# Performance work log

Hardware: AMD Instinct MI355X
Metric: run time of the kernel (lower is better)

## Reference

```python
import jax, jax.numpy as jnp
import numpy as np

B, L, D, H = 8, 1500, 1024, 8
HD = D // H
N_BOUNDARIES = 300  # exactly 300 boundaries per sequence -> max_segments = 300
EPS = 1e-5


def setup_inputs() -> dict:
    key = jax.random.key(0)
    ks = jax.random.split(key, 6)
    rng = np.random.default_rng(0)
    boundaries = np.zeros((B, L), dtype=np.float32)
    for b in range(B):
        boundaries[b, rng.permutation(L)[:N_BOUNDARIES]] = 1.0
    lengths = rng.uniform(0.5, 1.0, size=(B,)).astype(np.float32)
    hidden = jax.random.normal(ks[0], (B, L, D), jnp.float32)
    learned_query = jax.random.normal(ks[1], (D,), jnp.float32) * 0.02
    eye = jnp.eye(D, dtype=jnp.float32)
    # identity-initialized projections, perturbed so the test is non-trivial
    Wk = eye + 0.02 * jax.random.normal(ks[2], (D, D), jnp.float32)
    Wv = eye + 0.02 * jax.random.normal(ks[3], (D, D), jnp.float32)
    Wo = eye + 0.02 * jax.random.normal(ks[4], (D, D), jnp.float32)
    return {
        'hidden': hidden,
        'boundaries': jnp.asarray(boundaries),
        'lengths': jnp.asarray(lengths),
        'learned_query': learned_query,
        'Wk': Wk, 'Wv': Wv, 'Wo': Wo,
        'ln_gamma': jnp.ones((D,), jnp.float32),
        'ln_beta': jnp.zeros((D,), jnp.float32),
        'max_segments': N_BOUNDARIES,
    }


def _attention_pooling(hidden, boundaries, lengths, learned_query, Wk, Wv, Wo,
                       ln_gamma, ln_beta, max_segments):
    # segment id per token: cumsum(b) - b (token before first boundary -> seg 0)
    seg_id = jnp.cumsum(boundaries, axis=1) - boundaries            # (B, L)
    # foo[b,t,s] = s - seg_id[b,t]; foo == 0 -> token t belongs to segment s
    seg_mask = (jnp.arange(max_segments)[None, None, :] == seg_id[:, :, None])
    actual_lens = (lengths * L).astype(jnp.int32)                   # (B,)
    len_mask = jnp.arange(L)[None, :] < actual_lens[:, None]        # (B, L)
    seg_mask = seg_mask & len_mask[:, :, None]                      # (B, L, S) bool

    # LayerNorm (biased variance, as torch.nn.LayerNorm)
    mu = jnp.mean(hidden, axis=-1, keepdims=True)
    var = jnp.var(hidden, axis=-1, keepdims=True)
    hn = (hidden - mu) * jax.lax.rsqrt(var + EPS) * ln_gamma + ln_beta

    k = (hn @ Wk.T).reshape(B, L, H, HD)
    v = (hn @ Wv.T).reshape(B, L, H, HD)
    q = learned_query.reshape(H, HD)
    # queries are the same learned vector for every segment -> compute (B,H,L)
    # once and broadcast across S (same math as the original dense matmul)
    scores = jnp.einsum('hd,blhd->bhl', q, k) * (HD ** -0.5)        # (B, H, L)

    mask = seg_mask.transpose(0, 2, 1)[:, None, :, :]               # (B, 1, S, L)
    scores4 = jnp.where(mask, scores[:, :, None, :], -1e30)         # (B, H, S, L)
    w = jax.nn.softmax(scores4, axis=-1)
    w = jnp.where(mask, w, 0.0)
    # rows with no valid token: softmax of all -inf -> nan_to_num(0) in torch
    row_valid = jnp.any(mask, axis=-1, keepdims=True)
    w = jnp.where(row_valid, w, 0.0)

    pooled = jnp.einsum('bhsl,blhd->bshd', w, v).reshape(B, max_segments, D)
    return pooled @ Wo.T                                            # (B, S, D)


def reference(hidden, boundaries, lengths, learned_query, Wk, Wv, Wo,
              ln_gamma, ln_beta, max_segments):
    return _attention_pooling(hidden, boundaries, lengths, learned_query,
                              Wk, Wv, Wo, ln_gamma, ln_beta, max_segments)
```

## Files before the change

### kernel.cpp

```cpp
#include <hip/hip_runtime.h>
#include <hip/hip_bf16.h>

#define BPK_B 8
#define BPK_L 1500
#define BPK_D 1024
#define BPK_H 8
#define BPK_S 300
#define BPK_EPS 1e-5f
#define BPK_M (BPK_B * BPK_L)
#define BPK_MS (BPK_B * BPK_S)
#define BPK_MS_TILES 19
#define BPK_HP_ROWS 2432
#define BPK_PO_PAD 3072

typedef __hip_bfloat16 bf16;
typedef __bf16 bf16x8 __attribute__((ext_vector_type(8)));
typedef float v4f __attribute__((ext_vector_type(4)));

static __device__ __forceinline__ float bf_lo(unsigned u) {
    return __uint_as_float((u & 0xffffu) << 16);
}
static __device__ __forceinline__ float bf_hi(unsigned u) {
    return __uint_as_float((u >> 16) << 16);
}
static __device__ __forceinline__ void bpk_store(float v, float* p) { *p = v; }
static __device__ __forceinline__ void bpk_store(float v, bf16* p) { *p = __float2bfloat16(v); }
static __device__ __forceinline__ uint2 pack4bf(float a, float b, float c, float d) {
    union { bf16 h[4]; uint2 u; } pk;
    pk.h[0] = __float2bfloat16(a); pk.h[1] = __float2bfloat16(b);
    pk.h[2] = __float2bfloat16(c); pk.h[3] = __float2bfloat16(d);
    return pk.u;
}

#define BPK_GL2LDS(gsrc, ldst)                                                 \
    __builtin_amdgcn_global_load_lds(                                          \
        (const __attribute__((address_space(1))) void*)(gsrc),                 \
        (__attribute__((address_space(3))) void*)(ldst), 16, 0, 0)

__global__ __launch_bounds__(256) void bpk_prep_kernel(
    const float* __restrict__ Wv, const float* __restrict__ Wo,
    const float* __restrict__ lq, const float* __restrict__ Wk,
    const float* __restrict__ boundaries, const float* __restrict__ lengths,
    bf16* __restrict__ wvb, bf16* __restrict__ wob, bf16* __restrict__ qkb,
    int* __restrict__ seg_start, int* __restrict__ seg_cnt) {
    __shared__ unsigned char flags[1536];
    __shared__ int st_sh[BPK_S + 2];
    __shared__ int wsumi[4];
    int blk = blockIdx.x;
    int tid = threadIdx.x;
    if (blk < 2048) {
        const float* s = blk < 1024 ? Wv : Wo;
        bf16* d = blk < 1024 ? wvb : wob;
        int i = ((blk & 1023) * 256 + tid) * 4;
        float4 v = *(const float4*)(s + i);
        *(uint2*)(d + i) = pack4bf(v.x, v.y, v.z, v.w);
        return;
    }
    if (blk < 2080) {
        int o = (blk - 2048) * 256 + tid;
        int h = o >> 10, k = o & 1023;
        const float* wr = Wk + (size_t)(h * 128) * BPK_D + k;
        const float* qr = lq + h * 128;
        float s = 0.f;
        #pragma unroll 8
        for (int d = 0; d < 128; d++)
            s += qr[d] * wr[(size_t)d * BPK_D];
        qkb[o] = __float2bfloat16(s);
        return;
    }
    int b = blk - 2080;
    int alen = (int)(lengths[b] * (float)BPK_L);
    const float* bd = boundaries + (size_t)b * BPK_L;
    for (int t = tid; t < 1536; t += 256)
        flags[t] = (t < BPK_L && bd[t] >= 0.5f) ? 1 : 0;
    for (int s = tid; s < BPK_S + 2; s += 256) st_sh[s] = BPK_L;
    __syncthreads();
    int base = tid * 6;
    int lsum = 0;
    #pragma unroll
    for (int j = 0; j < 6; j++) lsum += flags[base + j];
    int lane = tid & 63, wid = tid >> 6;
    int scan = lsum;
    #pragma unroll
    for (int off = 1; off < 64; off <<= 1) {
        int u = __shfl_up(scan, off);
        if (lane >= off) scan += u;
    }
    if (lane == 63) wsumi[wid] = scan;
    __syncthreads();
    int wbase = 0;
    for (int w = 0; w < wid; w++) wbase += wsumi[w];
    int run = wbase + scan - lsum;
    #pragma unroll
    for (int j = 0; j < 6; j++) {
        int t = base + j;
        if (t < BPK_L) {
            int sid = run;
            if ((t == 0 || flags[t - 1]) && sid <= BPK_S) st_sh[sid] = t;
            if (flags[t]) run++;
        }
    }
    __syncthreads();
    for (int s = tid; s < BPK_S; s += 256) {
        int st = st_sh[s];
        int e = min(st_sh[s + 1], alen);
        int s0 = min(st, alen);
        seg_start[b * BPK_S + s] = st;
        seg_cnt[b * BPK_S + s] = max(0, e - s0);
    }
}

__global__ __launch_bounds__(256) void bpk_ln_score_kernel(
    const float* __restrict__ x, const float* __restrict__ gamma,
    const float* __restrict__ beta, const bf16* __restrict__ qkb,
    float2* __restrict__ murs, float* __restrict__ scores) {
    __shared__ bf16 qks[BPK_H * BPK_D];
    int tid = threadIdx.x;
    int lane = tid & 63, wid = tid >> 6;
    for (int i = tid; i < (BPK_H * BPK_D) / 8; i += 256)
        ((uint4*)qks)[i] = ((const uint4*)qkb)[i];
    float4 g[4], bb[4];
    #pragma unroll
    for (int j = 0; j < 4; j++) {
        g[j]  = *(const float4*)(gamma + j * 256 + lane * 4);
        bb[j] = *(const float4*)(beta + j * 256 + lane * 4);
    }
    __syncthreads();
    const int nwaves = gridDim.x * 4;
    for (int row = blockIdx.x * 4 + wid; row < BPK_M; row += nwaves) {
        const float* xr = x + (size_t)row * BPK_D;
        float4 f[4];
        float s = 0.f, sq = 0.f;
        #pragma unroll
        for (int j = 0; j < 4; j++) {
            f[j] = *(const float4*)(xr + j * 256 + lane * 4);
            s  += f[j].x + f[j].y + f[j].z + f[j].w;
            sq += f[j].x * f[j].x + f[j].y * f[j].y
                + f[j].z * f[j].z + f[j].w * f[j].w;
        }
        #pragma unroll
        for (int off = 1; off < 64; off <<= 1) {
            s  += __shfl_xor(s, off);
            sq += __shfl_xor(sq, off);
        }
        float mu = s * (1.0f / BPK_D);
        float var = sq * (1.0f / BPK_D) - mu * mu;
        float rs = rsqrtf(var + BPK_EPS);
        float hv[16];
        #pragma unroll
        for (int j = 0; j < 4; j++) {
            hv[j * 4 + 0] = (f[j].x - mu) * rs * g[j].x + bb[j].x;
            hv[j * 4 + 1] = (f[j].y - mu) * rs * g[j].y + bb[j].y;
            hv[j * 4 + 2] = (f[j].z - mu) * rs * g[j].z + bb[j].z;
            hv[j * 4 + 3] = (f[j].w - mu) * rs * g[j].w + bb[j].w;
        }
        float p[8];
        #pragma unroll
        for (int h = 0; h < 8; h++) {
            p[h] = 0.f;
            #pragma unroll
            for (int j = 0; j < 4; j++) {
                uint2 qv = *(const uint2*)(qks + h * BPK_D + j * 256 + lane * 4);
                p[h] += hv[j * 4 + 0] * bf_lo(qv.x) + hv[j * 4 + 1] * bf_hi(qv.x)
                      + hv[j * 4 + 2] * bf_lo(qv.y) + hv[j * 4 + 3] * bf_hi(qv.y);
            }
        }
        #pragma unroll
        for (int h = 0; h < 8; h++)
            #pragma unroll
            for (int off = 1; off < 64; off <<= 1)
                p[h] += __shfl_xor(p[h], off);
        if (lane < 8) {
            int b = row / BPK_L, t = row - b * BPK_L;
            scores[((size_t)b * BPK_H + lane) * BPK_L + t] =
                p[lane] * 0.088388347648318447f;
        } else if (lane == 8) {
            murs[row] = make_float2(mu, rs);
        }
    }
}

__global__ __launch_bounds__(256) void bpk_pool_kernel(
    const float* __restrict__ scores, const float* __restrict__ x,
    const float* __restrict__ gamma, const float* __restrict__ beta,
    const float2* __restrict__ murs,
    const int* __restrict__ seg_start, const int* __restrict__ seg_cnt,
    bf16* __restrict__ hpool) {
    int bs = blockIdx.x;
    int b = bs / BPK_S;
    int tid = threadIdx.x;
    int lane = tid & 63, wid = tid >> 6;
    __shared__ float minv[8][2];
    __shared__ float wls[8][128];
    int cnt = seg_cnt[bs], st = seg_start[bs];
    float4 g4 = *(const float4*)(gamma + tid * 4);
    float4 b4 = *(const float4*)(beta + tid * 4);
    float acc[8][4];
    #pragma unroll
    for (int h = 0; h < 8; h++)
        #pragma unroll
        for (int j = 0; j < 4; j++) acc[h][j] = 0.f;
    if (cnt > 0) {
        if (wid == 0) {
            int h = lane & 7, i0 = lane >> 3;
            const float* sc = scores + ((size_t)(b * 8 + h)) * BPK_L + st;
            float m = -1e30f;
            for (int i = i0; i < cnt; i += 8) m = fmaxf(m, sc[i]);
            #pragma unroll
            for (int off = 8; off < 64; off <<= 1) m = fmaxf(m, __shfl_xor(m, off));
            float l = 0.f;
            for (int i = i0; i < cnt; i += 8) l += __expf(sc[i] - m);
            #pragma unroll
            for (int off = 8; off < 64; off <<= 1) l += __shfl_xor(l, off);
            if (i0 == 0) { minv[h][0] = m; minv[h][1] = 1.0f / l; }
        }
        __syncthreads();
        for (int cb = 0; cb < cnt; cb += 128) {
            int cc = min(128, cnt - cb);
            int hh = tid >> 5, i0 = (tid & 31) * 4;
            #pragma unroll
            for (int j = 0; j < 4; j++) {
                int i = i0 + j;
                if (i < cc)
                    wls[hh][i] = __expf(scores[((size_t)(b * 8 + hh)) * BPK_L + st + cb + i]
                                        - minv[hh][0]) * minv[hh][1];
            }
            __syncthreads();
            const float* xp = x + (size_t)(b * BPK_L + st + cb) * BPK_D + tid * 4;
            const float2* mp = murs + (size_t)(b * BPK_L + st + cb);
            for (int i = 0; i < cc; i++) {
                float4 f = *(const float4*)(xp + (size_t)i * BPK_D);
                float2 mr = mp[i];
                float x0 = (f.x - mr.x) * mr.y * g4.x + b4.x;
                float x1 = (f.y - mr.x) * mr.y * g4.y + b4.y;
                float x2 = (f.z - mr.x) * mr.y * g4.z + b4.z;
                float x3 = (f.w - mr.x) * mr.y * g4.w + b4.w;
                #pragma unroll
                for (int h = 0; h < 8; h++) {
                    float w = wls[h][i];
                    acc[h][0] += w * x0; acc[h][1] += w * x1;
                    acc[h][2] += w * x2; acc[h][3] += w * x3;
                }
            }
            __syncthreads();
        }
    }
    #pragma unroll
    for (int h = 0; h < 8; h++)
        *(uint2*)(hpool + ((size_t)h * BPK_HP_ROWS + bs) * BPK_D + tid * 4) =
            pack4bf(acc[h][0], acc[h][1], acc[h][2], acc[h][3]);
}

__global__ __launch_bounds__(256) void bpk_headgemm_kernel(
    const bf16* __restrict__ hpool, const bf16* __restrict__ wvb,
    bf16* __restrict__ pooled) {
    const int mt = blockIdx.x, h = blockIdx.y;
    const int m0 = mt * 128;
    const bf16* A = hpool + (size_t)h * BPK_HP_ROWS * BPK_D;
    const bf16* W = wvb + (size_t)(h * 128) * BPK_D;
    __shared__ bf16 As[128][32];
    __shared__ bf16 Bs[128][32];
    const int tid = threadIdx.x;
    const int lane = tid & 63, wid = tid >> 6;
    const int wm = (wid & 1) * 64, wn = (wid >> 1) * 64;
    const int lm = lane & 15, quad = lane >> 4;
    const int c0 = wid * 2;
    const int rA = c0 * 16 + (lane >> 2);
    const int colc = (lane & 3) * 8;

    v4f acc[4][4];
    #pragma unroll
    for (int i = 0; i < 4; i++)
        #pragma unroll
        for (int j = 0; j < 4; j++) acc[i][j] = (v4f){0.f, 0.f, 0.f, 0.f};

    for (int k0 = 0; k0 < BPK_D; k0 += 32) {
        const bf16* pa = &A[(size_t)(m0 + rA) * BPK_D + k0 + colc];
        const bf16* pw = &W[(size_t)rA * BPK_D + k0 + colc];
        BPK_GL2LDS(pa, &As[c0 * 16][0]);
        BPK_GL2LDS(pa + (size_t)16 * BPK_D, &As[(c0 + 1) * 16][0]);
        BPK_GL2LDS(pw, &Bs[c0 * 16][0]);
        BPK_GL2LDS(pw + (size_t)16 * BPK_D, &Bs[(c0 + 1) * 16][0]);
        __syncthreads();
        bf16x8 af[4], bfr[4];
        #pragma unroll
        for (int i = 0; i < 4; i++)
            af[i] = *(const bf16x8*)&As[wm + i * 16 + lm][quad * 8];
        #pragma unroll
        for (int j = 0; j < 4; j++)
            bfr[j] = *(const bf16x8*)&Bs[wn + j * 16 + lm][quad * 8];
        #pragma unroll
        for (int i = 0; i < 4; i++)
            #pragma unroll
            for (int j = 0; j < 4; j++)
                acc[i][j] = __builtin_amdgcn_mfma_f32_16x16x32_bf16(af[i], bfr[j], acc[i][j], 0, 0, 0);
        __syncthreads();
    }
    #pragma unroll
    for (int i = 0; i < 4; i++) {
        int mbase = m0 + wm + i * 16 + quad * 4;
        #pragma unroll
        for (int j = 0; j < 4; j++) {
            int col = h * 128 + wn + j * 16 + lm;
            #pragma unroll
            for (int r = 0; r < 4; r++) {
                int m = mbase + r;
                if (m < BPK_MS)
                    pooled[(size_t)m * BPK_D + col] = __float2bfloat16(acc[i][j][r]);
            }
        }
    }
}

template <typename OT>
__global__ __launch_bounds__(256) void bpk_gemm_bt_kernel(
    const bf16* __restrict__ A, const bf16* __restrict__ W,
    OT* __restrict__ O, int M, int NT) {
    const int flat = blockIdx.x;
    const int xcd = flat & 7, slot = flat >> 3;
    const int mt = xcd + 8 * (slot / NT);
    const int nt = slot % NT;
    const int n0 = nt * 128;
    const int m0 = mt * 128;
    __shared__ bf16 As[128][32];
    __shared__ bf16 Bs[128][32];
    const int tid = threadIdx.x;
    const int lane = tid & 63, wid = tid >> 6;
    const int wm = (wid & 1) * 64, wn = (wid >> 1) * 64;
    const int lm = lane & 15, quad = lane >> 4;
    const int c0 = wid * 2;
    const int rA = c0 * 16 + (lane >> 2);
    const int colc = (lane & 3) * 8;

    v4f acc[4][4];
    #pragma unroll
    for (int i = 0; i < 4; i++)
        #pragma unroll
        for (int j = 0; j < 4; j++) acc[i][j] = (v4f){0.f, 0.f, 0.f, 0.f};

    for (int k0 = 0; k0 < BPK_D; k0 += 32) {
        const bf16* pa = &A[(size_t)(m0 + rA) * BPK_D + k0 + colc];
        const bf16* pw = &W[(size_t)(n0 + rA) * BPK_D + k0 + colc];
        BPK_GL2LDS(pa, &As[c0 * 16][0]);
        BPK_GL2LDS(pa + (size_t)16 * BPK_D, &As[(c0 + 1) * 16][0]);
        BPK_GL2LDS(pw, &Bs[c0 * 16][0]);
        BPK_GL2LDS(pw + (size_t)16 * BPK_D, &Bs[(c0 + 1) * 16][0]);
        __syncthreads();
        bf16x8 af[4], bfr[4];
        #pragma unroll
        for (int i = 0; i < 4; i++)
            af[i] = *(const bf16x8*)&As[wm + i * 16 + lm][quad * 8];
        #pragma unroll
        for (int j = 0; j < 4; j++)
            bfr[j] = *(const bf16x8*)&Bs[wn + j * 16 + lm][quad * 8];
        #pragma unroll
        for (int i = 0; i < 4; i++)
            #pragma unroll
            for (int j = 0; j < 4; j++)
                acc[i][j] = __builtin_amdgcn_mfma_f32_16x16x32_bf16(af[i], bfr[j], acc[i][j], 0, 0, 0);
        __syncthreads();
    }
    #pragma unroll
    for (int i = 0; i < 4; i++) {
        int mbase = m0 + wm + i * 16 + quad * 4;
        #pragma unroll
        for (int j = 0; j < 4; j++) {
            int col = n0 + wn + j * 16 + lm;
            #pragma unroll
            for (int r = 0; r < 4; r++) {
                int m = mbase + r;
                if (m < M) bpk_store(acc[i][j][r], &O[(size_t)m * BPK_D + col]);
            }
        }
    }
}

extern "C" void kernel_launch(void* const* d_in, const int* in_sizes, int n_in,
                              void* d_out, int out_size, void* d_ws, size_t ws_size,
                              hipStream_t stream) {
    const float* hidden     = (const float*)d_in[0];
    const float* boundaries = (const float*)d_in[1];
    const float* lengths    = (const float*)d_in[2];
    const float* lq         = (const float*)d_in[3];
    const float* Wk         = (const float*)d_in[4];
    const float* Wv         = (const float*)d_in[5];
    const float* Wo         = (const float*)d_in[6];
    const float* gamma      = (const float*)d_in[7];
    const float* beta       = (const float*)d_in[8];
    float* out              = (float*)d_out;

    char* ws = (char*)d_ws;
    size_t off = 0;
    auto carve = [&](size_t bytes) -> char* {
        char* p = ws + off;
        off += (bytes + 255) & ~(size_t)255;
        return p;
    };
    bf16* hpool    = (bf16*)carve((size_t)BPK_H * BPK_HP_ROWS * BPK_D * sizeof(bf16));
    bf16* pooled   = (bf16*)carve((size_t)BPK_PO_PAD * BPK_D * sizeof(bf16));
    bf16* wvb      = (bf16*)carve((size_t)BPK_D * BPK_D * sizeof(bf16));
    bf16* wob      = (bf16*)carve((size_t)BPK_D * BPK_D * sizeof(bf16));
    bf16* qkb      = (bf16*)carve((size_t)BPK_H * BPK_D * sizeof(bf16));
    float* scores  = (float*)carve((size_t)BPK_B * BPK_H * BPK_L * sizeof(float));
    float2* murs   = (float2*)carve((size_t)BPK_M * sizeof(float2));
    int* seg_start = (int*)carve((size_t)BPK_B * BPK_S * sizeof(int));
    int* seg_cnt   = (int*)carve((size_t)BPK_B * BPK_S * sizeof(int));

    bpk_prep_kernel<<<dim3(2088), dim3(256), 0, stream>>>(
        Wv, Wo, lq, Wk, boundaries, lengths, wvb, wob, qkb, seg_start, seg_cnt);
    bpk_ln_score_kernel<<<dim3(1024), dim3(256), 0, stream>>>(
        hidden, gamma, beta, qkb, murs, scores);
    bpk_pool_kernel<<<dim3(BPK_MS), dim3(256), 0, stream>>>(
        scores, hidden, gamma, beta, murs, seg_start, seg_cnt, hpool);
    bpk_headgemm_kernel<<<dim3(BPK_MS_TILES, BPK_H), dim3(256), 0, stream>>>(
        hpool, wvb, pooled);
    bpk_gemm_bt_kernel<float><<<dim3((BPK_PO_PAD / 128) * 8), dim3(256), 0, stream>>>(
        pooled, wob, out, BPK_MS, 8);
}
```

Baseline: 190.1 us.

## Skip masked rows, hold qk in registers, use butterfly reduce-scatter for scores

The LN+score kernel now skips tokens beyond each sequence's valid length, since those tokens never contribute to the pooled output. The query-key bf16 vectors are held in registers instead of being staged through shared memory, which removes a per-block shared copy and a barrier. The eight per-head wave reductions are replaced by a reduce-scatter butterfly that needs far fewer shuffles, with each head's result landing in a specific lane. This raises register pressure by 32 uint2 values per thread, and it relies on the pool kernel never reading scores or murs entries for the skipped tokens.

```diff
diff --git a/kernel.cpp b/kernel.cpp
--- a/kernel.cpp
+++ b/kernel.cpp
@@ -113,21 +113,33 @@
 __global__ __launch_bounds__(256) void bpk_ln_score_kernel(
     const float* __restrict__ x, const float* __restrict__ gamma,
     const float* __restrict__ beta, const bf16* __restrict__ qkb,
+    const float* __restrict__ lengths,
     float2* __restrict__ murs, float* __restrict__ scores) {
-    __shared__ bf16 qks[BPK_H * BPK_D];
     int tid = threadIdx.x;
     int lane = tid & 63, wid = tid >> 6;
-    for (int i = tid; i < (BPK_H * BPK_D) / 8; i += 256)
-        ((uint4*)qks)[i] = ((const uint4*)qkb)[i];
     float4 g[4], bb[4];
+    uint2 qk[8][4];
     #pragma unroll
     for (int j = 0; j < 4; j++) {
         g[j]  = *(const float4*)(gamma + j * 256 + lane * 4);
         bb[j] = *(const float4*)(beta + j * 256 + lane * 4);
     }
-    __syncthreads();
+    #pragma unroll
+    for (int h = 0; h < 8; h++)
+        #pragma unroll
+        for (int j = 0; j < 4; j++)
+            qk[h][j] = *(const uint2*)(qkb + h * BPK_D + j * 256 + lane * 4);
+    float lv = (lane < BPK_B) ? lengths[lane] : 0.f;
+    const bool b0 = (lane & 1) != 0;
+    const bool b1 = (lane & 2) != 0;
+    const bool b2 = (lane & 4) != 0;
+    const int head = 4 * (lane & 1) + (lane & 2) + ((lane >> 2) & 1);
+
     const int nwaves = gridDim.x * 4;
     for (int row = blockIdx.x * 4 + wid; row < BPK_M; row += nwaves) {
+        int b = row / BPK_L, t = row - b * BPK_L;
+        float alenf = __shfl(lv, b);
+        if (t >= (int)(alenf * (float)BPK_L)) continue;
         const float* xr = x + (size_t)row * BPK_D;
         float4 f[4];
         float s = 0.f, sq = 0.f;
@@ -146,34 +158,54 @@
         float mu = s * (1.0f / BPK_D);
         float var = sq * (1.0f / BPK_D) - mu * mu;
         float rs = rsqrtf(var + BPK_EPS);
-        float hv[16];
+        float p[8];
+        #pragma unroll
+        for (int h = 0; h < 8; h++) p[h] = 0.f;
         #pragma unroll
         for (int j = 0; j < 4; j++) {
-            hv[j * 4 + 0] = (f[j].x - mu) * rs * g[j].x + bb[j].x;
-            hv[j * 4 + 1] = (f[j].y - mu) * rs * g[j].y + bb[j].y;
-            hv[j * 4 + 2] = (f[j].z - mu) * rs * g[j].z + bb[j].z;
-            hv[j * 4 + 3] = (f[j].w - mu) * rs * g[j].w + bb[j].w;
-        }
-        float p[8];
-        #pragma unroll
-        for (int h = 0; h < 8; h++) {
-            p[h] = 0.f;
-            #pragma unroll
-            for (int j = 0; j < 4; j++) {
-                uint2 qv = *(const uint2*)(qks + h * BPK_D + j * 256 + lane * 4);
-                p[h] += hv[j * 4 + 0] * bf_lo(qv.x) + hv[j * 4 + 1] * bf_hi(qv.x)
-                      + hv[j * 4 + 2] * bf_lo(qv.y) + hv[j * 4 + 3] * bf_hi(qv.y);
+            float h0 = (f[j].x - mu) * rs * g[j].x + bb[j].x;
+            float h1 = (f[j].y - mu) * rs * g[j].y + bb[j].y;
+            float h2 = (f[j].z - mu) * rs * g[j].z + bb[j].z;
+            float h3 = (f[j].w - mu) * rs * g[j].w + bb[j].w;
+            #pragma unroll
+            for (int h = 0; h < 8; h++) {
+                uint2 qv = qk[h][j];
+                p[h] += h0 * bf_lo(qv.x) + h1 * bf_hi(qv.x)
+                      + h2 * bf_lo(qv.y) + h3 * bf_hi(qv.y);
             }
         }
         #pragma unroll
-        for (int h = 0; h < 8; h++)
-            #pragma unroll
-            for (int off = 1; off < 64; off <<= 1)
-                p[h] += __shfl_xor(p[h], off);
+        for (int r = 0; r < 4; r++) {
+            float send = b0 ? p[r] : p[r + 4];
+            float recv = __shfl_xor(send, 1);
+            p[r]     += b0 ? 0.f : recv;
+            p[r + 4] += b0 ? recv : 0.f;
+        }
+        float q0 = b0 ? p[4] : p[0];
+        float q1 = b0 ? p[5] : p[1];
+        float q2 = b0 ? p[6] : p[2];
+        float q3 = b0 ? p[7] : p[3];
+        {
+            float send = b1 ? q0 : q2;
+            float recv = __shfl_xor(send, 2);
+            q0 += b1 ? 0.f : recv;
+            q2 += b1 ? recv : 0.f;
+            send = b1 ? q1 : q3;
+            recv = __shfl_xor(send, 2);
+            q1 += b1 ? 0.f : recv;
+            q3 += b1 ? recv : 0.f;
+        }
+        float a = b1 ? q2 : q0;
+        float c = b1 ? q3 : q1;
+        float send = b2 ? a : c;
+        float recv = __shfl_xor(send, 4);
+        float v = (b2 ? c : a) + recv;
+        v += __shfl_xor(v, 8);
+        v += __shfl_xor(v, 16);
+        v += __shfl_xor(v, 32);
         if (lane < 8) {
-            int b = row / BPK_L, t = row - b * BPK_L;
-            scores[((size_t)b * BPK_H + lane) * BPK_L + t] =
-                p[lane] * 0.088388347648318447f;
+            scores[((size_t)b * BPK_H + head) * BPK_L + t] =
+                v * 0.088388347648318447f;
         } else if (lane == 8) {
             murs[row] = make_float2(mu, rs);
         }
@@ -409,7 +441,7 @@
     bpk_prep_kernel<<<dim3(2088), dim3(256), 0, stream>>>(
         Wv, Wo, lq, Wk, boundaries, lengths, wvb, wob, qkb, seg_start, seg_cnt);
     bpk_ln_score_kernel<<<dim3(1024), dim3(256), 0, stream>>>(
-        hidden, gamma, beta, qkb, murs, scores);
+        hidden, gamma, beta, qkb, lengths, murs, scores);
     bpk_pool_kernel<<<dim3(BPK_MS), dim3(256), 0, stream>>>(
         scores, hidden, gamma, beta, murs, seg_start, seg_cnt, hpool);
     bpk_headgemm_kernel<<<dim3(BPK_MS_TILES, BPK_H), dim3(256), 0, stream>>>(
```

After: 191.7 us. No clear change (+0.8%).
